# Kernel tuning notes

Measured on AMD Instinct MI355X. Metric: run time of the kernel, lower is better.

The kernel has to match this reference:

```python
import jax, jax.numpy as jnp
import numpy as np

H, W, HEADS, DIM_HEAD, SLICE = 256, 256, 8, 64, 64
SCALE = DIM_HEAD ** -0.5


def _conv(x_nhwc, w_hwio, b):
    y = jax.lax.conv_general_dilated(
        x_nhwc, w_hwio, window_strides=(1, 1), padding='SAME',
        dimension_numbers=('NHWC', 'HWIO', 'NHWC'))
    return y + b


def setup_inputs() -> dict:
    key = jax.random.key(0)
    ks = jax.random.split(key, 13)
    B, N, C, inner = 2, H * W, 128, HEADS * DIM_HEAD
    s = lambda k, shp, sc: jax.random.normal(k, shp, jnp.float32) * sc
    return {
        'x': s(ks[0], (B, N, C), 1.0),
        'Wfx': s(ks[1], (3, 3, C, inner), 0.05),
        'bfx': s(ks[2], (inner,), 0.02),
        'Wx': s(ks[3], (3, 3, C, inner), 0.05),
        'bx': s(ks[4], (inner,), 0.02),
        'Wslice': s(ks[5], (SLICE, DIM_HEAD), 0.1),
        'bslice': s(ks[6], (SLICE,), 0.02),
        'temperature': jnp.ones((1, HEADS, 1, 1), jnp.float32) * 0.5,
        'Wq': s(ks[7], (DIM_HEAD, DIM_HEAD), 0.1),
        'Wk': s(ks[8], (DIM_HEAD, DIM_HEAD), 0.1),
        'Wv': s(ks[9], (DIM_HEAD, DIM_HEAD), 0.1),
        'Wout': s(ks[10], (C, inner), 0.05),
        'bout': s(ks[11], (C,), 0.02),
    }


def reference(x, Wfx, bfx, Wx, bx, Wslice, bslice, temperature, Wq, Wk, Wv, Wout, bout):
    B, N, C = x.shape
    xg = x.reshape(B, H, W, C)                       # NHWC grid
    # conv QKV-style projections -> [B, heads, N, dim_head]
    def to_heads(y):
        return y.reshape(B, N, HEADS, DIM_HEAD).transpose(0, 2, 1, 3)
    fx_mid = to_heads(_conv(xg, Wfx, bfx))           # [B,h,N,d]
    x_mid = to_heads(_conv(xg, Wx, bx))              # [B,h,N,d]
    # slice assignment weights: softmax over slices with clamped temperature
    temp = jnp.clip(temperature, 0.1, 5.0)           # [1,h,1,1]
    logits = (jnp.einsum('bhnd,gd->bhng', x_mid, Wslice) + bslice) / temp
    slice_weights = jax.nn.softmax(logits, axis=-1)  # [B,h,N,G]
    slice_norm = slice_weights.sum(axis=2)           # [B,h,G]
    slice_token = jnp.einsum('bhnc,bhng->bhgc', fx_mid, slice_weights)
    slice_token = slice_token / (slice_norm + 1e-5)[..., None]  # [B,h,G,d]
    # small attention over slice tokens
    q = jnp.einsum('bhgd,ed->bhge', slice_token, Wq)
    k = jnp.einsum('bhgd,ed->bhge', slice_token, Wk)
    v = jnp.einsum('bhgd,ed->bhge', slice_token, Wv)
    attn = jax.nn.softmax(jnp.einsum('bhge,bhfe->bhgf', q, k) * SCALE, axis=-1)
    out_slice = jnp.einsum('bhgf,bhfe->bhge', attn, v)           # [B,h,G,d]
    # scatter back to tokens
    out_x = jnp.einsum('bhgc,bhng->bhnc', out_slice, slice_weights)
    out_x = out_x.transpose(0, 2, 1, 3).reshape(B, N, HEADS * DIM_HEAD)
    return jnp.einsum('bni,oi->bno', out_x, Wout) + bout
```

## Files before the change

### kernel.cpp

```cpp
#include <hip/hip_runtime.h>


typedef _Float16 f16;
typedef _Float16 f16x8 __attribute__((ext_vector_type(8)));
typedef float    f32x4 __attribute__((ext_vector_type(4)));

static const size_t OFF_PADX = 0;
static const size_t OFF_WCAT = 17040384;
static const size_t OFF_ST   = 19399680;
static const size_t OFF_NORM = 19530752;
static const size_t OFF_OS   = 19532800;
static const size_t OFF_PT   = 19663872;
static const size_t OFF_XMID = 19794944;
static const size_t OFF_FXT  = 86903808;

__device__ __forceinline__ void ldsdma16(f16* lds, const f16* g) {
  __builtin_amdgcn_global_load_lds((__attribute__((address_space(1))) void*)g,
                                   (__attribute__((address_space(3))) void*)lds,
                                   16, 0, 0);
}

__global__ __launch_bounds__(256) void pad_kernel(const float* __restrict__ xb,
                                                  f16* __restrict__ padx) {
  int idx = blockIdx.x * 256 + threadIdx.x;
  if (idx >= 258 * 258 * 16) return;
  int c8 = (idx & 15) * 8;
  int r  = idx >> 4;
  int jp = r % 258;
  int ip = r / 258;
  f16x8 v;
  if (ip == 0 || ip == 257 || jp == 0 || jp == 257) {
#pragma unroll
    for (int j = 0; j < 8; ++j) v[j] = (f16)0.0f;
  } else {
    const float* src = xb + ((size_t)(ip - 1) * 256 + (jp - 1)) * 128 + c8;
#pragma unroll
    for (int j = 0; j < 8; ++j) v[j] = (f16)src[j];
  }
  *(f16x8*)(padx + (size_t)r * 128 + c8) = v;
}

__global__ __launch_bounds__(256) void prepw_kernel(const float* __restrict__ Wfx,
                                                    const float* __restrict__ Wx,
                                                    f16* __restrict__ wcat) {
  int idx = blockIdx.x * 256 + threadIdx.x;
  if (idx >= 9 * 1024 * 128) return;
  int ci = idx & 127;
  int t  = idx >> 7;
  int co = t & 1023;
  int tap = t >> 10;
  float v = (co < 512) ? Wfx[(size_t)(tap * 128 + ci) * 512 + co]
                       : Wx[(size_t)(tap * 128 + ci) * 512 + (co - 512)];
  wcat[idx] = (f16)v;
}

__global__ __launch_bounds__(256, 2) void conv_kernel(const f16* __restrict__ padx,
                                                      const f16* __restrict__ wcat,
                                                      const float* __restrict__ bfx,
                                                      const float* __restrict__ bx,
                                                      f16* __restrict__ xmid,
                                                      f16* __restrict__ fxT) {
  __shared__ f16 As[128 * 64];
  __shared__ f16 Bs[128 * 64];
  int tid = threadIdx.x;
  int nt = blockIdx.x & 7;
  int mt = blockIdx.x >> 3;
  int i  = mt >> 1;
  int j0 = (mt & 1) * 128;
  int n0 = nt * 128;
  int lane = tid & 63, wave = tid >> 6;
  int ln15 = lane & 15, quad = lane >> 4;
  int wm = wave & 1, wn = wave >> 1;

  int rr[4], qq8[4];
#pragma unroll
  for (int ph = 0; ph < 4; ++ph) {
    int s = ph * 256 + tid;
    rr[ph] = s >> 3;
    qq8[ph] = ((s & 7) ^ (rr[ph] & 7)) * 8;
  }
  int wbase = wave * 512;

  f32x4 acc[4][4] = {};

  for (int di = 0; di < 3; ++di) {
    for (int dj = 0; dj < 3; ++dj) {
      const f16* aBase = padx + ((size_t)(i + di) * 258 + (j0 + dj)) * 128;
      const f16* bBase = wcat + ((size_t)((di * 3 + dj) * 1024 + n0)) * 128;
      for (int kc = 0; kc < 128; kc += 64) {
#pragma unroll
        for (int ph = 0; ph < 4; ++ph) {
          ldsdma16(&As[ph * 2048 + wbase], aBase + (size_t)rr[ph] * 128 + kc + qq8[ph]);
          ldsdma16(&Bs[ph * 2048 + wbase], bBase + (size_t)rr[ph] * 128 + kc + qq8[ph]);
        }
        __syncthreads();
#pragma unroll
        for (int ks = 0; ks < 2; ++ks) {
          f16x8 af[4], bfr[4];
          int q = ks * 4 + quad;
#pragma unroll
          for (int xx = 0; xx < 4; ++xx) {
            int ra = wm * 64 + xx * 16 + ln15;
            int rb = wn * 64 + xx * 16 + ln15;
            af[xx]  = *(const f16x8*)(&As[ra * 64 + (q ^ (ra & 7)) * 8]);
            bfr[xx] = *(const f16x8*)(&Bs[rb * 64 + (q ^ (rb & 7)) * 8]);
          }
#pragma unroll
          for (int mf = 0; mf < 4; ++mf)
#pragma unroll
            for (int nf = 0; nf < 4; ++nf)
              acc[mf][nf] = __builtin_amdgcn_mfma_f32_16x16x32_f16(af[mf], bfr[nf],
                                                                   acc[mf][nf], 0, 0, 0);
        }
        __syncthreads();
      }
    }
  }

  size_t token0 = (size_t)i * 256 + j0;
#pragma unroll
  for (int nf = 0; nf < 4; ++nf) {
    int col = n0 + wn * 64 + nf * 16 + ln15;
    float bias = (col < 512) ? bfx[col] : bx[col - 512];
#pragma unroll
    for (int mf = 0; mf < 4; ++mf) {
      int rbase = wm * 64 + mf * 16 + quad * 4;
#pragma unroll
      for (int v = 0; v < 4; ++v) {
        int token = token0 + rbase + v;
        f16 val = (f16)(acc[mf][nf][v] + bias);
        if (col < 512) fxT[(size_t)col * 65536 + token] = val;
        else           xmid[(size_t)token * 512 + (col - 512)] = val;
      }
    }
  }
}

#define WS_S 72
#define WT_S 264
__global__ __launch_bounds__(256, 2) void slice_kernel(f16* __restrict__ xmid,
                                                       const f16* __restrict__ fxT,
                                                       const float* __restrict__ Wslice,
                                                       const float* __restrict__ bslice,
                                                       const float* __restrict__ temperature,
                                                       float* __restrict__ ST,
                                                       float* __restrict__ snorm) {
  __shared__ f16 Ws[64 * WS_S];
  __shared__ f16 Wt[64 * WT_S];
  __shared__ float red[64 * 65];
  __shared__ float redn[64];
  int tid = threadIdx.x;
  int h = blockIdx.x >> 6;
  int chunk = blockIdx.x & 63;
  int tok0 = chunk * 1024;
  int lane = tid & 63, wave = tid >> 6;
  int ln15 = lane & 15, quad = lane >> 4;

  for (int s = tid; s < 4096; s += 256)
    Ws[(s >> 6) * WS_S + (s & 63)] = (f16)Wslice[s];
  if (tid < 64) redn[tid] = 0.f;
  float tc = temperature[h];
  tc = fminf(fmaxf(tc, 0.1f), 5.0f);
  float invt = 1.0f / tc;
  float bsv[4];
#pragma unroll
  for (int nf = 0; nf < 4; ++nf) bsv[nf] = bslice[nf * 16 + ln15];
  __syncthreads();

  f32x4 acc2[4][4] = {};
  float naccv[4] = {};

  for (int it = 0; it < 4; ++it) {
    int tsub = it * 256 + wave * 64;
    f32x4 accA[4][4] = {};
#pragma unroll
    for (int kq = 0; kq < 2; ++kq) {
      f16x8 bf[4];
#pragma unroll
      for (int nf = 0; nf < 4; ++nf)
        bf[nf] = *(const f16x8*)(&Ws[(nf * 16 + ln15) * WS_S + kq * 32 + quad * 8]);
#pragma unroll
      for (int mf = 0; mf < 4; ++mf) {
        f16x8 af = *(const f16x8*)(xmid + (size_t)(tok0 + tsub + mf * 16 + ln15) * 512 +
                                   h * 64 + kq * 32 + quad * 8);
#pragma unroll
        for (int nf = 0; nf < 4; ++nf)
          accA[mf][nf] = __builtin_amdgcn_mfma_f32_16x16x32_f16(af, bf[nf], accA[mf][nf],
                                                                0, 0, 0);
      }
    }
#pragma unroll
    for (int mf = 0; mf < 4; ++mf) {
#pragma unroll
      for (int v = 0; v < 4; ++v) {
        float l[4];
#pragma unroll
        for (int nf = 0; nf < 4; ++nf) l[nf] = (accA[mf][nf][v] + bsv[nf]) * invt;
        float lm = fmaxf(fmaxf(l[0], l[1]), fmaxf(l[2], l[3]));
#pragma unroll
        for (int off = 1; off < 16; off <<= 1) lm = fmaxf(lm, __shfl_xor(lm, off, 64));
        float e[4], ssum = 0.f;
#pragma unroll
        for (int nf = 0; nf < 4; ++nf) { e[nf] = __expf(l[nf] - lm); ssum += e[nf]; }
#pragma unroll
        for (int off = 1; off < 16; off <<= 1) ssum += __shfl_xor(ssum, off, 64);
        float winv = 1.0f / ssum;
        int t_loc = tsub + mf * 16 + quad * 4 + v;
        int t_str = wave * 64 + mf * 16 + quad * 4 + v;
        f16* wrow = xmid + (size_t)(tok0 + t_loc) * 512 + h * 64;
#pragma unroll
        for (int nf = 0; nf < 4; ++nf) {
          float w = e[nf] * winv;
          naccv[nf] += w;
          f16 wh = (f16)w;
          wrow[nf * 16 + ln15] = wh;
          Wt[(nf * 16 + ln15) * WT_S + t_str] = wh;
        }
      }
    }
#pragma unroll
    for (int kq = 0; kq < 2; ++kq) {
      int kof = wave * 64 + kq * 32 + quad * 8;
      f16x8 bfB[4];
#pragma unroll
      for (int nf = 0; nf < 4; ++nf)
        bfB[nf] = *(const f16x8*)(fxT + (size_t)(h * 64 + nf * 16 + ln15) * 65536 +
                                  tok0 + it * 256 + kof);
#pragma unroll
      for (int mf = 0; mf < 4; ++mf) {
        f16x8 afB = *(const f16x8*)(&Wt[(mf * 16 + ln15) * WT_S + kof]);
#pragma unroll
        for (int nf = 0; nf < 4; ++nf)
          acc2[mf][nf] = __builtin_amdgcn_mfma_f32_16x16x32_f16(afB, bfB[nf],
                                                                acc2[mf][nf], 0, 0, 0);
      }
    }
  }

#pragma unroll
  for (int nf = 0; nf < 4; ++nf) atomicAdd(&redn[nf * 16 + ln15], naccv[nf]);

  for (int s = 0; s < 4; ++s) {
    if (wave == s) {
#pragma unroll
      for (int mf = 0; mf < 4; ++mf)
#pragma unroll
        for (int nf = 0; nf < 4; ++nf)
#pragma unroll
          for (int v = 0; v < 4; ++v) {
            int g = mf * 16 + quad * 4 + v;
            int d = nf * 16 + ln15;
            if (s == 0) red[g * 65 + d] = acc2[mf][nf][v];
            else        red[g * 65 + d] += acc2[mf][nf][v];
          }
    }
    __syncthreads();
  }
  float* stp = ST + (size_t)h * 4096;
  for (int s2 = tid; s2 < 4096; s2 += 256)
    atomicAdd(&stp[s2], red[(s2 >> 6) * 65 + (s2 & 63)]);
  if (tid < 64) atomicAdd(&snorm[h * 64 + tid], redn[tid]);
}

__global__ __launch_bounds__(256) void attn_kernel(const float* __restrict__ ST,
                                                   const float* __restrict__ snorm,
                                                   const float* __restrict__ Wq,
                                                   const float* __restrict__ Wk,
                                                   const float* __restrict__ Wv,
                                                   float* __restrict__ OS) {
  int h = blockIdx.x;
  __shared__ float tok[64 * 65];
  __shared__ float qs[64 * 65];
  __shared__ float ksm[64 * 65];
  __shared__ f16 vsm[64 * 65];
  int tid = threadIdx.x;
  const float* stp = ST + (size_t)h * 4096;
  const float* snp = snorm + (size_t)h * 64;
  for (int s = tid; s < 4096; s += 256) {
    int g = s >> 6, d = s & 63;
    tok[g * 65 + d] = stp[s] / (snp[g] + 1e-5f);
  }
  __syncthreads();
  int g = tid >> 2, p16 = (tid & 3) * 16;
  for (int e0 = 0; e0 < 16; ++e0) {
    int e = p16 + e0;
    const float* wq = Wq + e * 64;
    const float* wk = Wk + e * 64;
    const float* wv = Wv + e * 64;
    float aq = 0, ak = 0, av = 0;
#pragma unroll 8
    for (int d = 0; d < 64; ++d) {
      float tv = tok[g * 65 + d];
      aq += tv * wq[d];
      ak += tv * wk[d];
      av += tv * wv[d];
    }
    qs[g * 65 + e] = aq;
    ksm[g * 65 + e] = ak;
    vsm[g * 65 + e] = (f16)av;
  }
  __syncthreads();
  float* sc = tok;
  for (int f0 = 0; f0 < 16; ++f0) {
    int f = p16 + f0;
    float s = 0;
#pragma unroll 8
    for (int e = 0; e < 64; ++e) s += qs[g * 65 + e] * ksm[f * 65 + e];
    sc[g * 65 + f] = s * 0.125f;
  }
  __syncthreads();
  if (tid < 64) {
    float m = -1e30f;
    for (int f = 0; f < 64; ++f) m = fmaxf(m, sc[tid * 65 + f]);
    float ssum = 0;
    for (int f = 0; f < 64; ++f) {
      float e = __expf(sc[tid * 65 + f] - m);
      sc[tid * 65 + f] = e;
      ssum += e;
    }
    float inv = 1.0f / ssum;
    for (int f = 0; f < 64; ++f) sc[tid * 65 + f] *= inv;
  }
  __syncthreads();
  for (int e0 = 0; e0 < 16; ++e0) {
    int e = p16 + e0;
    float o = 0;
#pragma unroll 8
    for (int f = 0; f < 64; ++f) o += sc[g * 65 + f] * (float)vsm[f * 65 + e];
    OS[(size_t)h * 4096 + g * 64 + e] = o;
  }
}

__global__ __launch_bounds__(256) void pt_kernel(const float* __restrict__ OS,
                                                 const float* __restrict__ Wout,
                                                 f16* __restrict__ PT) {
  int h = blockIdx.x;
  __shared__ float os[64 * 65];
  int tid = threadIdx.x;
  for (int s = tid; s < 4096; s += 256) os[(s >> 6) * 65 + (s & 63)] = OS[(size_t)h * 4096 + s];
  __syncthreads();
  int o = tid >> 1, gh = (tid & 1) * 32;
  const float* wr = Wout + (size_t)o * 512 + h * 64;
  float wreg[64];
#pragma unroll
  for (int d = 0; d < 64; ++d) wreg[d] = wr[d];
  for (int gg = 0; gg < 32; ++gg) {
    int g = gh + gg;
    float s = 0;
#pragma unroll
    for (int d = 0; d < 64; ++d) s += os[g * 65 + d] * wreg[d];
    PT[(size_t)o * 512 + h * 64 + g] = (f16)s;
  }
}

__global__ __launch_bounds__(256, 2) void final_kernel(const f16* __restrict__ xmid,
                                                       const f16* __restrict__ PT,
                                                       const float* __restrict__ bout,
                                                       float* __restrict__ outb) {
  __shared__ f16 As[128 * 64];
  __shared__ f16 Bs[128 * 64];
  int tid = threadIdx.x;
  int tok0 = blockIdx.x << 7;
  int lane = tid & 63, wave = tid >> 6;
  int ln15 = lane & 15, quad = lane >> 4;
  int wm = wave & 1, wn = wave >> 1;
  int rr[4], qq8[4];
#pragma unroll
  for (int ph = 0; ph < 4; ++ph) {
    int s = ph * 256 + tid;
    rr[ph] = s >> 3;
    qq8[ph] = ((s & 7) ^ (rr[ph] & 7)) * 8;
  }
  int wbase = wave * 512;
  f32x4 acc[4][4] = {};
  const f16* aB = xmid + (size_t)tok0 * 512;
  const f16* bB = PT;
  for (int kc = 0; kc < 512; kc += 64) {
#pragma unroll
    for (int ph = 0; ph < 4; ++ph) {
      ldsdma16(&As[ph * 2048 + wbase], aB + (size_t)rr[ph] * 512 + kc + qq8[ph]);
      ldsdma16(&Bs[ph * 2048 + wbase], bB + (size_t)rr[ph] * 512 + kc + qq8[ph]);
    }
    __syncthreads();
#pragma unroll
    for (int ks = 0; ks < 2; ++ks) {
      f16x8 af[4], bfr[4];
      int q = ks * 4 + quad;
#pragma unroll
      for (int xx = 0; xx < 4; ++xx) {
        int ra = wm * 64 + xx * 16 + ln15;
        int rb = wn * 64 + xx * 16 + ln15;
        af[xx]  = *(const f16x8*)(&As[ra * 64 + (q ^ (ra & 7)) * 8]);
        bfr[xx] = *(const f16x8*)(&Bs[rb * 64 + (q ^ (rb & 7)) * 8]);
      }
#pragma unroll
      for (int mf = 0; mf < 4; ++mf)
#pragma unroll
        for (int nf = 0; nf < 4; ++nf)
          acc[mf][nf] = __builtin_amdgcn_mfma_f32_16x16x32_f16(af[mf], bfr[nf],
                                                               acc[mf][nf], 0, 0, 0);
    }
    __syncthreads();
  }
#pragma unroll
  for (int nf = 0; nf < 4; ++nf) {
    int col = wn * 64 + nf * 16 + ln15;
    float bo = bout[col];
#pragma unroll
    for (int mf = 0; mf < 4; ++mf) {
      int rbase = wm * 64 + mf * 16 + quad * 4;
#pragma unroll
      for (int v = 0; v < 4; ++v)
        outb[(size_t)(tok0 + rbase + v) * 128 + col] = acc[mf][nf][v] + bo;
    }
  }
}

extern "C" void kernel_launch(void* const* d_in, const int* in_sizes, int n_in,
                              void* d_out, int out_size, void* d_ws, size_t ws_size,
                              hipStream_t stream) {
  const float* x    = (const float*)d_in[0];
  const float* Wfx  = (const float*)d_in[1];
  const float* bfx  = (const float*)d_in[2];
  const float* Wx   = (const float*)d_in[3];
  const float* bx   = (const float*)d_in[4];
  const float* Wsl  = (const float*)d_in[5];
  const float* bsl  = (const float*)d_in[6];
  const float* temp = (const float*)d_in[7];
  const float* Wq   = (const float*)d_in[8];
  const float* Wk   = (const float*)d_in[9];
  const float* Wv   = (const float*)d_in[10];
  const float* Wout = (const float*)d_in[11];
  const float* bout = (const float*)d_in[12];
  float* out = (float*)d_out;
  char* ws = (char*)d_ws;

  f16*  padx = (f16*)(ws + OFF_PADX);
  f16*  wcat = (f16*)(ws + OFF_WCAT);
  float* ST  = (float*)(ws + OFF_ST);
  float* nrm = (float*)(ws + OFF_NORM);
  float* OS  = (float*)(ws + OFF_OS);
  f16*  PT   = (f16*)(ws + OFF_PT);
  f16*  xmid = (f16*)(ws + OFF_XMID);
  f16*  fxT  = (f16*)(ws + OFF_FXT);

  prepw_kernel<<<4608, 256, 0, stream>>>(Wfx, Wx, wcat);
  for (int b = 0; b < 2; ++b) {
    const float* xb = x + (size_t)b * 65536 * 128;
    float* outb = out + (size_t)b * 65536 * 128;
    hipMemsetAsync(ws + OFF_ST, 0, 131072 + 2048, stream);
    pad_kernel<<<4161, 256, 0, stream>>>(xb, padx);
    conv_kernel<<<4096, 256, 0, stream>>>(padx, wcat, bfx, bx, xmid, fxT);
    slice_kernel<<<512, 256, 0, stream>>>(xmid, fxT, Wsl, bsl, temp, ST, nrm);
    attn_kernel<<<8, 256, 0, stream>>>(ST, nrm, Wq, Wk, Wv, OS);
    pt_kernel<<<8, 256, 0, stream>>>(OS, Wout, PT);
    final_kernel<<<512, 256, 0, stream>>>(xmid, PT, bout, outb);
  }
}
```

Before: 1.027 ms.

## Reuse the conv input row tile across horizontal taps and raise occupancy target

The conv kernel now loads a 130-row activation tile once per vertical tap and chunk of 64 input channels. It reuses that tile for all three horizontal taps by shifting the row index, instead of reloading a 128-row A tile for every tap. Weight tiles for two taps are loaded together into a doubled B buffer, and the third tap gets its own load, which cuts the number of barrier rounds. The launch-bounds occupancy hint rises from 2 to 3 blocks per CU. This adds shared memory per block and puts more register pressure on the MFMA accumulators, which could cause spills.

```diff
diff --git a/kernel.cpp b/kernel.cpp
--- a/kernel.cpp
+++ b/kernel.cpp
@@ -54,14 +54,14 @@
   wcat[idx] = (f16)v;
 }
 
-__global__ __launch_bounds__(256, 2) void conv_kernel(const f16* __restrict__ padx,
+__global__ __launch_bounds__(256, 3) void conv_kernel(const f16* __restrict__ padx,
                                                       const f16* __restrict__ wcat,
                                                       const float* __restrict__ bfx,
                                                       const float* __restrict__ bx,
                                                       f16* __restrict__ xmid,
                                                       f16* __restrict__ fxT) {
-  __shared__ f16 As[128 * 64];
-  __shared__ f16 Bs[128 * 64];
+  __shared__ f16 As[130 * 64];
+  __shared__ f16 Bs[2 * 128 * 64];
   int tid = threadIdx.x;
   int nt = blockIdx.x & 7;
   int mt = blockIdx.x >> 3;
@@ -72,38 +72,43 @@
   int ln15 = lane & 15, quad = lane >> 4;
   int wm = wave & 1, wn = wave >> 1;
 
-  int rr[4], qq8[4];
-#pragma unroll
-  for (int ph = 0; ph < 4; ++ph) {
-    int s = ph * 256 + tid;
-    rr[ph] = s >> 3;
-    qq8[ph] = ((s & 7) ^ (rr[ph] & 7)) * 8;
-  }
-  int wbase = wave * 512;
-
   f32x4 acc[4][4] = {};
 
   for (int di = 0; di < 3; ++di) {
-    for (int dj = 0; dj < 3; ++dj) {
-      const f16* aBase = padx + ((size_t)(i + di) * 258 + (j0 + dj)) * 128;
-      const f16* bBase = wcat + ((size_t)((di * 3 + dj) * 1024 + n0)) * 128;
-      for (int kc = 0; kc < 128; kc += 64) {
-#pragma unroll
-        for (int ph = 0; ph < 4; ++ph) {
-          ldsdma16(&As[ph * 2048 + wbase], aBase + (size_t)rr[ph] * 128 + kc + qq8[ph]);
-          ldsdma16(&Bs[ph * 2048 + wbase], bBase + (size_t)rr[ph] * 128 + kc + qq8[ph]);
+    const f16* aRow = padx + ((size_t)(i + di) * 258 + j0) * 128;
+    for (int kc = 0; kc < 128; kc += 64) {
+#pragma unroll
+      for (int ph = 0; ph < 5; ++ph) {
+        int s = ph * 256 + tid;
+        if (s < 1040) {
+          int rr = s >> 3;
+          int qq = ((s & 7) ^ (rr & 7)) * 8;
+          ldsdma16(&As[(ph * 256 + wave * 64) * 8], aRow + (size_t)rr * 128 + kc + qq);
         }
-        __syncthreads();
+      }
+#pragma unroll
+      for (int ph = 0; ph < 8; ++ph) {
+        int s2 = ph * 256 + tid;
+        int dj = s2 >> 10;
+        int sB = s2 & 1023;
+        int rr = sB >> 3;
+        int qq = ((sB & 7) ^ (rr & 7)) * 8;
+        ldsdma16(&Bs[(ph * 256 + wave * 64) * 8],
+                 wcat + ((size_t)((di * 3 + dj) * 1024 + n0 + rr)) * 128 + kc + qq);
+      }
+      __syncthreads();
+#pragma unroll
+      for (int dj = 0; dj < 2; ++dj) {
 #pragma unroll
         for (int ks = 0; ks < 2; ++ks) {
+          int q = ks * 4 + quad;
           f16x8 af[4], bfr[4];
-          int q = ks * 4 + quad;
 #pragma unroll
           for (int xx = 0; xx < 4; ++xx) {
-            int ra = wm * 64 + xx * 16 + ln15;
+            int t  = dj + wm * 64 + xx * 16 + ln15;
             int rb = wn * 64 + xx * 16 + ln15;
-            af[xx]  = *(const f16x8*)(&As[ra * 64 + (q ^ (ra & 7)) * 8]);
-            bfr[xx] = *(const f16x8*)(&Bs[rb * 64 + (q ^ (rb & 7)) * 8]);
+            af[xx]  = *(const f16x8*)(&As[t * 64 + ((q ^ (t & 7)) * 8)]);
+            bfr[xx] = *(const f16x8*)(&Bs[dj * 8192 + rb * 64 + ((q ^ (rb & 7)) * 8)]);
           }
 #pragma unroll
           for (int mf = 0; mf < 4; ++mf)
@@ -112,8 +117,36 @@
               acc[mf][nf] = __builtin_amdgcn_mfma_f32_16x16x32_f16(af[mf], bfr[nf],
                                                                    acc[mf][nf], 0, 0, 0);
         }
-        __syncthreads();
-      }
+      }
+      __syncthreads();
+#pragma unroll
+      for (int ph = 0; ph < 4; ++ph) {
+        int sB = ph * 256 + tid;
+        int rr = sB >> 3;
+        int qq = ((sB & 7) ^ (rr & 7)) * 8;
+        ldsdma16(&Bs[(ph * 256 + wave * 64) * 8],
+                 wcat + ((size_t)((di * 3 + 2) * 1024 + n0 + rr)) * 128 + kc + qq);
+      }
+      __syncthreads();
+#pragma unroll
+      for (int ks = 0; ks < 2; ++ks) {
+        int q = ks * 4 + quad;
+        f16x8 af[4], bfr[4];
+#pragma unroll
+        for (int xx = 0; xx < 4; ++xx) {
+          int t  = 2 + wm * 64 + xx * 16 + ln15;
+          int rb = wn * 64 + xx * 16 + ln15;
+          af[xx]  = *(const f16x8*)(&As[t * 64 + ((q ^ (t & 7)) * 8)]);
+          bfr[xx] = *(const f16x8*)(&Bs[rb * 64 + ((q ^ (rb & 7)) * 8)]);
+        }
+#pragma unroll
+        for (int mf = 0; mf < 4; ++mf)
+#pragma unroll
+          for (int nf = 0; nf < 4; ++nf)
+            acc[mf][nf] = __builtin_amdgcn_mfma_f32_16x16x32_f16(af[mf], bfr[nf],
+                                                                 acc[mf][nf], 0, 0, 0);
+      }
+      __syncthreads();
     }
   }
 
```

After: 1.129 ms. 9.9% more time.
